# Kernel optimization log

Hardware: AMD Instinct MI355X
Metric: run time of the kernel (lower is better)

The kernel has to match this reference:

```python
import jax, jax.numpy as jnp
from jax import lax
import numpy as np

STATE_DIM = 64
CHANNELS = 128
SEQ_LEN = 4096
BATCH = 16
DT_MIN, DT_MAX = 1e-3, 1e-1


def hippo(n):
    # HiPPO-LegS construction, matching the torch staticmethod
    ar = jnp.arange(n, dtype=jnp.float32)
    P = jnp.sqrt(1.0 + 2.0 * ar)
    A = P[:, None] * P[None, :]
    A = jnp.tril(A) - jnp.diag(ar)
    B = jnp.sqrt(2.0 * ar + 1.0)
    return -A, B[:, None]


def setup_inputs() -> dict:
    key = jax.random.key(0)
    k_u, k_c = jax.random.split(key)
    A, B = hippo(STATE_DIM)
    # xavier_normal_ for C: std = sqrt(2/(fan_in+fan_out))
    std = float(np.sqrt(2.0 / (CHANNELS + STATE_DIM)))
    C = jax.random.normal(k_c, (CHANNELS, STATE_DIM), dtype=jnp.float32) * std
    D = jnp.ones((CHANNELS, 1), dtype=jnp.float32)
    # deterministic dt at log-midpoint of [dt_min, dt_max]
    dt = jnp.exp(jnp.array([(np.log(DT_MIN) + np.log(DT_MAX)) / 2.0], dtype=jnp.float32))
    u = jax.random.normal(k_u, (BATCH, SEQ_LEN), dtype=jnp.float32)
    return {"u": u, "A": A, "B": B, "C": C, "D": D, "dt": dt}


def reference(u, A, B, C, D, dt):
    # Training-path forward of LinearStateSpaceLayer (conv-kernel construction + conv1d)
    b, L = u.shape
    n = A.shape[0]
    dt_s = dt[0]
    I = jnp.eye(n, dtype=A.dtype)
    BL = jnp.linalg.inv(I - 0.5 * dt_s * A)            # bilinear discretization
    A_bar = BL @ (I + 0.5 * dt_s * A)                  # (n, n)
    B_bar = (BL * dt_s) @ B                            # (n, 1)

    # kernel k[j] = C @ A_bar^j @ B_bar for j = 0..L-1, via a scan of matvecs
    def step(v, _):
        return A_bar @ v, v
    _, vs = lax.scan(step, B_bar[:, 0], None, length=L)  # (L, n), vs[j] = A_bar^j B_bar
    k_causal = vs @ C.T                                  # (L, channels)
    # torch ordering: k_conv[c, 0, i] = C A_bar^{L-1-i} B_bar = k_causal[L-1-i, c]
    k_conv = k_causal[::-1].T[:, None, :]                # (channels, 1, L)

    # torch F.conv1d is cross-correlation; lax conv_general_dilated matches
    y = lax.conv_general_dilated(
        u[:, None, :], k_conv,
        window_strides=(1,), padding=[(L - 1, L - 1)],
        dimension_numbers=("NCH", "OIH", "NCH"),
    )[:, :, :L]                                          # (b, channels, L)

    # skip term: (u.unsqueeze(-1) @ D.T).transpose(-1,-2) == u[b,t] * D[c,0]
    y = y + u[:, None, :] * D[None, :, :]                # (b, channels, L)
    return y
```

## Files before the change

kernel.cpp:

```cpp
#include <hip/hip_runtime.h>

#define NS   64
#define CH   128
#define LSEQ 4096
#define NB   16
#define SCH  64
#define MCH  64
#define ST   68
#define CP   128

#define WS_ABAR 0
#define WS_A16  4096
#define WS_VS   8192
#define WS_BBAR 12288

#define X0_IDX(b, m) (((size_t)(b) * CH) * LSEQ + (size_t)(m) * SCH)

#define P_VSS  0
#define P_XCW  1024
#define P_XBS  1280
#define P_PLE  1536
#define P_PART 1792
#define P_A16  2048

#define FMA44(av, bv)                                                          \
    a0.x += av.x * bv.x; a0.y += av.x * bv.y; a0.z += av.x * bv.z; a0.w += av.x * bv.w; \
    a1.x += av.y * bv.x; a1.y += av.y * bv.y; a1.z += av.y * bv.z; a1.w += av.y * bv.w; \
    a2.x += av.z * bv.x; a2.y += av.z * bv.y; a2.z += av.z * bv.z; a2.w += av.z * bv.w; \
    a3.x += av.w * bv.x; a3.y += av.w * bv.y; a3.z += av.w * bv.z; a3.w += av.w * bv.w;


template<bool WT>
__device__ __forceinline__ void mm_square(const float* __restrict__ cm,
                                          const float* __restrict__ cmt,
                                          float* __restrict__ nm,
                                          float* __restrict__ nmt, int e) {
    const int l = e & 63;
    const int si0 = 16 * ((e >> 6) & 3) + 4 * (l >> 4);
    const int sj0 = 4 * (l & 15);
    const int kmax = si0 + 4;
    float4 a0 = {0,0,0,0}, a1 = {0,0,0,0}, a2 = {0,0,0,0}, a3 = {0,0,0,0};
    for (int k = 0; k < kmax; k += 4) {
        float4 av0 = *(const float4*)&cmt[(k + 0) * ST + si0];
        float4 bv0 = *(const float4*)&cm [(k + 0) * ST + sj0];
        float4 av1 = *(const float4*)&cmt[(k + 1) * ST + si0];
        float4 bv1 = *(const float4*)&cm [(k + 1) * ST + sj0];
        float4 av2 = *(const float4*)&cmt[(k + 2) * ST + si0];
        float4 bv2 = *(const float4*)&cm [(k + 2) * ST + sj0];
        float4 av3 = *(const float4*)&cmt[(k + 3) * ST + si0];
        float4 bv3 = *(const float4*)&cm [(k + 3) * ST + sj0];
        FMA44(av0, bv0)
        FMA44(av1, bv1)
        FMA44(av2, bv2)
        FMA44(av3, bv3)
    }
    *(float4*)&nm[(si0 + 0) * ST + sj0] = a0;
    *(float4*)&nm[(si0 + 1) * ST + sj0] = a1;
    *(float4*)&nm[(si0 + 2) * ST + sj0] = a2;
    *(float4*)&nm[(si0 + 3) * ST + sj0] = a3;
    if (WT) {
        float4 t0 = {a0.x, a1.x, a2.x, a3.x};
        float4 t1 = {a0.y, a1.y, a2.y, a3.y};
        float4 t2 = {a0.z, a1.z, a2.z, a3.z};
        float4 t3 = {a0.w, a1.w, a2.w, a3.w};
        *(float4*)&nmt[(sj0 + 0) * ST + si0] = t0;
        *(float4*)&nmt[(sj0 + 1) * ST + si0] = t1;
        *(float4*)&nmt[(sj0 + 2) * ST + si0] = t2;
        *(float4*)&nmt[(sj0 + 3) * ST + si0] = t3;
    }
}

__device__ __forceinline__ void mm_sq42(const float* __restrict__ cm,
                                        const float* __restrict__ cmt,
                                        float* __restrict__ nm,
                                        float* __restrict__ nmt, int tid) {
    const int si0 = 4 * (tid >> 5);
    const int sj0 = 2 * (tid & 31);
    const int kmax = si0 + 4;
    float2 a0 = {0,0}, a1 = {0,0}, a2 = {0,0}, a3 = {0,0};
#pragma unroll 4
    for (int k = 0; k < kmax; ++k) {
        float4 av = *(const float4*)&cmt[k * ST + si0];
        float2 bv = *(const float2*)&cm [k * ST + sj0];
        a0.x += av.x * bv.x; a0.y += av.x * bv.y;
        a1.x += av.y * bv.x; a1.y += av.y * bv.y;
        a2.x += av.z * bv.x; a2.y += av.z * bv.y;
        a3.x += av.w * bv.x; a3.y += av.w * bv.y;
    }
    *(float2*)&nm[(si0 + 0) * ST + sj0] = a0;
    *(float2*)&nm[(si0 + 1) * ST + sj0] = a1;
    *(float2*)&nm[(si0 + 2) * ST + sj0] = a2;
    *(float2*)&nm[(si0 + 3) * ST + sj0] = a3;
    float4 t0 = {a0.x, a1.x, a2.x, a3.x};
    float4 t1 = {a0.y, a1.y, a2.y, a3.y};
    *(float4*)&nmt[(sj0 + 0) * ST + si0] = t0;
    *(float4*)&nmt[(sj0 + 1) * ST + si0] = t1;
}

__device__ __forceinline__ void vs_expand1(const float* __restrict__ cmt,
                                           float* __restrict__ VT,
                                           int iq, int j, int mexp) {
    const int i0 = 4 * iq;
    float4 acc = {0,0,0,0};
#pragma unroll 8
    for (int k = 0; k < NS; ++k) {
        float4 av = *(const float4*)&cmt[k * ST + i0];
        float bk = VT[k * ST + j];
        acc.x += av.x * bk; acc.y += av.y * bk;
        acc.z += av.z * bk; acc.w += av.w * bk;
    }
    VT[(i0 + 0) * ST + mexp + j] = acc.x;
    VT[(i0 + 1) * ST + mexp + j] = acc.y;
    VT[(i0 + 2) * ST + mexp + j] = acc.z;
    VT[(i0 + 3) * ST + mexp + j] = acc.w;
}

__device__ __forceinline__ void pq_step(const float* __restrict__ Acol,
                                        const float* __restrict__ xle,
                                        float* __restrict__ outb, int r0, int e) {
    const int g = e >> 4, i0 = 4 * (e & 15);
    const float* bp = &xle[(4 * g + r0) * NS];
    float4 acc = *(const float4*)&xle[(4 * g + r0 + 1) * NS + i0];
#pragma unroll 8
    for (int k = 0; k < NS; ++k) {
        float4 av = *(const float4*)&Acol[k * ST + i0];
        float bk = bp[k];
        acc.x = fmaf(av.x, bk, acc.x); acc.y = fmaf(av.y, bk, acc.y);
        acc.z = fmaf(av.z, bk, acc.z); acc.w = fmaf(av.w, bk, acc.w);
    }
    *(float4*)&outb[g * ST + i0] = acc;
}

__device__ __forceinline__ void y_step512(const float* __restrict__ A128col,
                                          const float* __restrict__ P,
                                          const float* __restrict__ Q,
                                          float* __restrict__ Y, int e) {
    const int g = e >> 5, c0 = 2 * (e & 31);
    const float* bp = &P[g * ST];
    float2 acc = *(const float2*)&Q[g * ST + c0];
#pragma unroll 8
    for (int k = 0; k < NS; ++k) {
        float2 av = *(const float2*)&A128col[k * ST + c0];
        float bk = bp[k];
        acc.x = fmaf(av.x, bk, acc.x); acc.y = fmaf(av.y, bk, acc.y);
    }
    *(float2*)&Y[g * ST + c0] = acc;
}

__device__ __forceinline__ void inner_step(const float* __restrict__ Acol,
                                           const float* __restrict__ xle,
                                           float* __restrict__ stash, int r, int e) {
    const int g = e >> 4, i0 = 4 * (e & 15);
    const int mp = 4 * g + r - 1;
    float4 acc = *(const float4*)&xle[mp * NS + i0];
    const float* xp = &stash[mp * ST];
#pragma unroll 8
    for (int k = 0; k < NS; ++k) {
        float4 av = *(const float4*)&Acol[k * ST + i0];
        float xk = xp[k];
        acc.x = fmaf(av.x, xk, acc.x); acc.y = fmaf(av.y, xk, acc.y);
        acc.z = fmaf(av.z, xk, acc.z); acc.w = fmaf(av.w, xk, acc.w);
    }
    *(float4*)&stash[(mp + 1) * ST + i0] = acc;
}

__device__ __forceinline__ void inner512(const float* __restrict__ Acol,
                                         const float* __restrict__ xle,
                                         float* __restrict__ stash, int r, int e) {
    const int g = e >> 5, c0 = 2 * (e & 31);
    const int mp = 4 * g + r - 1;
    float2 acc = *(const float2*)&xle[mp * NS + c0];
    const float* xp = &stash[mp * ST];
#pragma unroll 8
    for (int k = 0; k < NS; ++k) {
        float2 av = *(const float2*)&Acol[k * ST + c0];
        float xk = xp[k];
        acc.x = fmaf(av.x, xk, acc.x); acc.y = fmaf(av.y, xk, acc.y);
    }
    *(float2*)&stash[(mp + 1) * ST + c0] = acc;
}

__device__ __forceinline__ void e1u_step(const float* __restrict__ A128col,
                                         const float* __restrict__ P,
                                         float* __restrict__ stash, int e) {
    const int g = e >> 4, i0 = 4 * (e & 15);
    const float* xp = &stash[(4 * g) * ST];
    float4 acc = *(const float4*)&P[g * ST + i0];
#pragma unroll 8
    for (int k = 0; k < NS; ++k) {
        float4 av = *(const float4*)&A128col[k * ST + i0];
        float xk = xp[k];
        acc.x = fmaf(av.x, xk, acc.x); acc.y = fmaf(av.y, xk, acc.y);
        acc.z = fmaf(av.z, xk, acc.z); acc.w = fmaf(av.w, xk, acc.w);
    }
    *(float4*)&stash[(4 * g + 2) * ST + i0] = acc;
}

__global__ __launch_bounds__(512) void k_sb(const float* __restrict__ u,
                                            const float* __restrict__ A,
                                            const float* __restrict__ Bv,
                                            const float* __restrict__ dtp,
                                            float* __restrict__ ws,
                                            float* __restrict__ out) {
    __shared__ __align__(16) float Mrow[NS * ST];
    __shared__ __align__(16) float Mcol[(NS + 1) * ST];
    __shared__ __align__(16) float Nrow[NS * ST];
    __shared__ __align__(16) float Ncol[NS * ST];
    __shared__ __align__(16) float VT[NS * ST];
    __shared__ __align__(16) float uT[NS * ST];
    __shared__ __align__(16) float vsS[NS * NS];
    __shared__ __align__(16) float xleS[MCH * NS];
    __shared__ __align__(16) float bcol[NS];
    __shared__ float rdiag[NS], xcS[NS];
    float* const stash = uT;
    float* const HbP = vsS;
    float* const HbQ = vsS + 16 * ST;
    float* const HbY = vsS + 32 * ST;
    const int tid = threadIdx.x;
    const int b = blockIdx.x;
    const float dt = dtp[0];
    const float hdt = 0.5f * dt;

    for (int o = tid; o < NS * NS; o += 512) {
        int i = o >> 6, k = o & 63;
        float a = A[o];
        float d = (i == k) ? 1.0f : 0.0f;
        Nrow[i * ST + k] = d - hdt * a;
        Ncol[k * ST + i] = d + hdt * a;
    }
    if (tid < NS) {
        bcol[tid]  = dt * Bv[tid];
        rdiag[tid] = 1.0f / (1.0f - hdt * A[tid * NS + tid]);
    }
    __syncthreads();

    {
        const int jj = tid & 63;
#pragma unroll
        for (int rep = 0; rep < 2; ++rep) {
            const int m0 = 4 * (tid >> 6) + 32 * rep;
            float4 v;
            v.x = u[b * LSEQ + (m0 + 0) * SCH + 63 - jj];
            v.y = u[b * LSEQ + (m0 + 1) * SCH + 63 - jj];
            v.z = u[b * LSEQ + (m0 + 2) * SCH + 63 - jj];
            v.w = u[b * LSEQ + (m0 + 3) * SCH + 63 - jj];
            *(float4*)&uT[jj * ST + m0] = v;
        }
    }

    if (tid <= NS) {
        float xr[NS];
        const float* t2b = (tid < NS) ? &Ncol[tid * ST] : bcol;
#pragma unroll
        for (int I = 0; I < 16; ++I) {
            const int i0 = 4 * I;
            float4 t2 = *(const float4*)&t2b[i0];
            float a0 = t2.x, a1 = t2.y, a2 = t2.z, a3 = t2.w;
#pragma unroll
            for (int k = 0; k < i0; k += 4) {
                float4 n0 = *(const float4*)&Nrow[(i0 + 0) * ST + k];
                float4 n1 = *(const float4*)&Nrow[(i0 + 1) * ST + k];
                float4 n2 = *(const float4*)&Nrow[(i0 + 2) * ST + k];
                float4 n3 = *(const float4*)&Nrow[(i0 + 3) * ST + k];
                a0 -= n0.x * xr[k] + n0.y * xr[k + 1] + n0.z * xr[k + 2] + n0.w * xr[k + 3];
                a1 -= n1.x * xr[k] + n1.y * xr[k + 1] + n1.z * xr[k + 2] + n1.w * xr[k + 3];
                a2 -= n2.x * xr[k] + n2.y * xr[k + 1] + n2.z * xr[k + 2] + n2.w * xr[k + 3];
                a3 -= n3.x * xr[k] + n3.y * xr[k + 1] + n3.z * xr[k + 2] + n3.w * xr[k + 3];
            }
            float4 rd  = *(const float4*)&rdiag[i0];
            float4 nb1 = *(const float4*)&Nrow[(i0 + 1) * ST + i0];
            float4 nb2 = *(const float4*)&Nrow[(i0 + 2) * ST + i0];
            float4 nb3 = *(const float4*)&Nrow[(i0 + 3) * ST + i0];
            float x0 = a0 * rd.x;
            float x1 = (a1 - nb1.x * x0) * rd.y;
            float x2 = (a2 - nb2.x * x0 - nb2.y * x1) * rd.z;
            float x3 = (a3 - nb3.x * x0 - nb3.y * x1 - nb3.z * x2) * rd.w;
            xr[i0 + 0] = x0; xr[i0 + 1] = x1; xr[i0 + 2] = x2; xr[i0 + 3] = x3;
        }
        float* xrow = &Mcol[tid * ST];
#pragma unroll
        for (int k = 0; k < NS; k += 4) {
            float4 v = {xr[k], xr[k + 1], xr[k + 2], xr[k + 3]};
            *(float4*)&xrow[k] = v;
        }
    }
    __syncthreads();

    if (tid < 256) {
        const int i0 = 4 * (tid >> 4), j0 = 4 * (tid & 15);
        float4 r0 = *(const float4*)&Mcol[(j0 + 0) * ST + i0];
        float4 r1 = *(const float4*)&Mcol[(j0 + 1) * ST + i0];
        float4 r2 = *(const float4*)&Mcol[(j0 + 2) * ST + i0];
        float4 r3 = *(const float4*)&Mcol[(j0 + 3) * ST + i0];
        float4 w0 = {r0.x, r1.x, r2.x, r3.x};
        float4 w1 = {r0.y, r1.y, r2.y, r3.y};
        float4 w2 = {r0.z, r1.z, r2.z, r3.z};
        float4 w3 = {r0.w, r1.w, r2.w, r3.w};
        *(float4*)&Mrow[(i0 + 0) * ST + j0] = w0;
        *(float4*)&Mrow[(i0 + 1) * ST + j0] = w1;
        *(float4*)&Mrow[(i0 + 2) * ST + j0] = w2;
        *(float4*)&Mrow[(i0 + 3) * ST + j0] = w3;
        if (b == 0) {
            *(float4*)&ws[WS_ABAR + (i0 + 0) * NS + j0] = w0;
            *(float4*)&ws[WS_ABAR + (i0 + 1) * NS + j0] = w1;
            *(float4*)&ws[WS_ABAR + (i0 + 2) * NS + j0] = w2;
            *(float4*)&ws[WS_ABAR + (i0 + 3) * NS + j0] = w3;
        }
    }
    if (b == 1 && tid < 16)
        *(float4*)&ws[WS_BBAR + 4 * tid] = *(const float4*)&Mcol[NS * ST + 4 * tid];
    if (tid < NS) VT[tid * ST + 0] = Mcol[NS * ST + tid];
    __syncthreads();

    float *cm = Mrow, *cmt = Mcol, *nm = Nrow, *nmt = Ncol;
    for (int s = 1; s <= 6; ++s) {
        if (s <= 4) {
            mm_sq42(cm, cmt, nm, nmt, tid);
            const int mexp = 1 << (s - 1);
            if (tid < 16 * mexp) {
                vs_expand1(cmt, VT, tid & 15, tid >> 4, mexp);
            }
        } else if (tid < 256) {
            mm_square<true>(cm, cmt, nm, nmt, tid);
        } else {
            const int e = tid - 256;
            const int iq = e & 15;
            if (s == 5) {
                vs_expand1(cmt, VT, iq, e >> 4, 16);
            } else {
                const int j0 = 2 * (e >> 4);
                const int i0 = 4 * iq;
                float4 c0 = {0,0,0,0}, c1 = {0,0,0,0};
#pragma unroll 8
                for (int k = 0; k < NS; ++k) {
                    float4 av = *(const float4*)&cmt[k * ST + i0];
                    float2 bv = *(const float2*)&VT[k * ST + j0];
                    c0.x += av.x * bv.x; c0.y += av.y * bv.x;
                    c0.z += av.z * bv.x; c0.w += av.w * bv.x;
                    c1.x += av.x * bv.y; c1.y += av.y * bv.y;
                    c1.z += av.z * bv.y; c1.w += av.w * bv.y;
                }
                float2 w0 = {c0.x, c1.x}, w1 = {c0.y, c1.y};
                float2 w2 = {c0.z, c1.z}, w3 = {c0.w, c1.w};
                *(float2*)&VT[(i0 + 0) * ST + 32 + j0] = w0;
                *(float2*)&VT[(i0 + 1) * ST + 32 + j0] = w1;
                *(float2*)&VT[(i0 + 2) * ST + 32 + j0] = w2;
                *(float2*)&VT[(i0 + 3) * ST + 32 + j0] = w3;
            }
        }
        __syncthreads();
        { float* t = cm; cm = nm; nm = t; t = cmt; cmt = nmt; nmt = t; }
        if (s == 4 && b == 2) {
            for (int o = tid; o < (NS * NS) / 4; o += 512) {
                int r = o >> 4, c4 = (o & 15) * 4;
                *(float4*)&ws[WS_A16 + r * NS + c4] = *(const float4*)&cm[r * ST + c4];
            }
        }
    }

    if (tid < 256) {
        const int i0 = 4 * (tid >> 4), j0 = 4 * (tid & 15);
        float4 v0 = *(const float4*)&VT[(i0 + 0) * ST + j0];
        float4 v1 = *(const float4*)&VT[(i0 + 1) * ST + j0];
        float4 v2 = *(const float4*)&VT[(i0 + 2) * ST + j0];
        float4 v3 = *(const float4*)&VT[(i0 + 3) * ST + j0];
        float4 w0 = {v0.x, v1.x, v2.x, v3.x};
        float4 w1 = {v0.y, v1.y, v2.y, v3.y};
        float4 w2 = {v0.z, v1.z, v2.z, v3.z};
        float4 w3 = {v0.w, v1.w, v2.w, v3.w};
        *(float4*)&vsS[(j0 + 0) * NS + i0] = w0;
        *(float4*)&vsS[(j0 + 1) * NS + i0] = w1;
        *(float4*)&vsS[(j0 + 2) * NS + i0] = w2;
        *(float4*)&vsS[(j0 + 3) * NS + i0] = w3;
        if (b == 3) {
            *(float4*)&ws[WS_VS + (j0 + 0) * NS + i0] = w0;
            *(float4*)&ws[WS_VS + (j0 + 1) * NS + i0] = w1;
            *(float4*)&ws[WS_VS + (j0 + 2) * NS + i0] = w2;
            *(float4*)&ws[WS_VS + (j0 + 3) * NS + i0] = w3;
        }
    } else {
        mm_square<true>(Mrow, Mcol, Nrow, Ncol, tid - 256);
    }
    __syncthreads();

    if (tid < 256) {
        const int ig = tid & 15, mg = tid >> 4;
        float4 a0 = {0,0,0,0}, a1 = {0,0,0,0}, a2 = {0,0,0,0}, a3 = {0,0,0,0};
#pragma unroll 4
        for (int j = 0; j < NS; j += 2) {
            float4 am  = *(const float4*)&uT[j * ST + 4 * mg];
            float4 bi  = *(const float4*)&vsS[j * NS + 4 * ig];
            float4 am2 = *(const float4*)&uT[(j + 1) * ST + 4 * mg];
            float4 bi2 = *(const float4*)&vsS[(j + 1) * NS + 4 * ig];
            FMA44(am, bi)
            FMA44(am2, bi2)
        }
        *(float4*)&xleS[(4 * mg + 0) * NS + 4 * ig] = a0;
        *(float4*)&xleS[(4 * mg + 1) * NS + 4 * ig] = a1;
        *(float4*)&xleS[(4 * mg + 2) * NS + 4 * ig] = a2;
        *(float4*)&xleS[(4 * mg + 3) * NS + 4 * ig] = a3;
    } else {
        mm_square<false>(Nrow, Ncol, VT, VT, tid - 256);
    }
    __syncthreads();

    if (tid < 256) pq_step(Mcol, xleS, HbP, 0, tid);
    else           pq_step(Mcol, xleS, HbQ, 2, tid - 256);
    if (tid < 64) { xcS[tid] = 0.f; stash[tid] = 0.f; }
    __syncthreads();

    y_step512(Ncol, HbP, HbQ, HbY, tid);
    __syncthreads();

    if (tid < 64) {
        const int i = tid;
        float4 arow[16];
#pragma unroll
        for (int c = 0; c < 16; ++c)
            arow[c] = *(const float4*)&VT[i * ST + 4 * c];
        float yv[15];
#pragma unroll
        for (int g = 0; g < 15; ++g) yv[g] = HbY[g * ST + i];
        for (int g = 0; g < 15; ++g) {
            float a0 = 0.f, a1 = 0.f, a2 = 0.f, a3 = 0.f;
#pragma unroll
            for (int c = 0; c < 16; ++c) {
                float4 xv = *(const float4*)&xcS[4 * c];
                a0 = fmaf(arow[c].x, xv.x, a0);
                a1 = fmaf(arow[c].y, xv.y, a1);
                a2 = fmaf(arow[c].z, xv.z, a2);
                a3 = fmaf(arow[c].w, xv.w, a3);
            }
            const float xn = ((a0 + a1) + (a2 + a3)) + yv[g];
            xcS[i] = xn;
            stash[(4 * g + 4) * ST + i] = xn;
        }
    }
    __syncthreads();

    if (tid < 256) inner_step(Mcol, xleS, stash, 1, tid);
    else           e1u_step(Ncol, HbP, stash, tid - 256);
    __syncthreads();

    inner512(Mcol, xleS, stash, 3, tid);
    __syncthreads();

    {
        const int m = tid >> 3, t8 = (tid & 7) * 8;
        float4 o1 = *(const float4*)&stash[m * ST + t8];
        float4 o2 = *(const float4*)&stash[m * ST + t8 + 4];
        *(float4*)&out[X0_IDX(b, m) + t8]     = o1;
        *(float4*)&out[X0_IDX(b, m) + t8 + 4] = o2;
    }
}

__global__ __launch_bounds__(256) void k_main2(const float* __restrict__ u,
                                               const float* __restrict__ Cm,
                                               const float* __restrict__ Dv,
                                               const float* __restrict__ ws,
                                               float* __restrict__ out) {
    __shared__ __align__(16) float Xl[NS * ST];
    __shared__ __align__(16) float pool[NS * CP];
    __shared__ float uS[SCH], DS[CH], bbS[NS];
    const int m = blockIdx.x, b = blockIdx.y;
    const int tid = threadIdx.x;
    const int l = tid & 63, w = tid >> 6;

    for (int o = tid; o < (NS * NS) / 4; o += 256) {
        int r = o >> 4, c4 = (o & 15) * 4;
        *(float4*)&Xl[r * ST + c4]          = *(const float4*)&ws[WS_ABAR + r * NS + c4];
        *(float4*)&pool[P_A16 + r * NS + c4] = *(const float4*)&ws[WS_A16 + r * NS + c4];
    }
    for (int o = tid; o < 16 * NS; o += 256) pool[P_VSS + o] = ws[WS_VS + o];
    if (tid < NS) {
        uS[tid]  = u[b * LSEQ + m * SCH + tid];
        bbS[tid] = ws[WS_BBAR + tid];
        pool[P_XBS + tid] = out[X0_IDX(b, m) + tid];
    }
    if (tid < CH) DS[tid] = Dv[tid];
    __syncthreads();

    float4 arow[16];
#pragma unroll
    for (int c = 0; c < 16; ++c)
        arow[c] = *(const float4*)&Xl[l * ST + 4 * c];
    const float bbl = bbS[l];
    float ur[16];
#pragma unroll
    for (int s = 0; s < 16; ++s) ur[s] = uS[16 * w + s];
    float4 a16r[4];
#pragma unroll
    for (int kq = 0; kq < 4; ++kq)
        a16r[kq] = *(const float4*)&pool[P_A16 + l * NS + 16 * w + 4 * kq];

    {
        float s = 0.f;
#pragma unroll
        for (int j = 0; j < 16; ++j) s += pool[P_VSS + j * NS + l] * uS[16 * w + 15 - j];
        pool[P_PLE + w * NS + l] = s;
    }
    __syncthreads();

    for (int p = 1; p < 4; ++p) {
        float4 x0q = *(const float4*)&pool[P_XBS + (p - 1) * NS + 16 * w + 0];
        float4 x1q = *(const float4*)&pool[P_XBS + (p - 1) * NS + 16 * w + 4];
        float4 x2q = *(const float4*)&pool[P_XBS + (p - 1) * NS + 16 * w + 8];
        float4 x3q = *(const float4*)&pool[P_XBS + (p - 1) * NS + 16 * w + 12];
        float s = a16r[0].x * x0q.x + a16r[0].y * x0q.y + a16r[0].z * x0q.z + a16r[0].w * x0q.w
                + a16r[1].x * x1q.x + a16r[1].y * x1q.y + a16r[1].z * x1q.z + a16r[1].w * x1q.w
                + a16r[2].x * x2q.x + a16r[2].y * x2q.y + a16r[2].z * x2q.z + a16r[2].w * x2q.w
                + a16r[3].x * x3q.x + a16r[3].y * x3q.y + a16r[3].z * x3q.z + a16r[3].w * x3q.w;
        pool[P_PART + w * NS + l] = s;
        __syncthreads();
        if (w == 0) {
            float xn = pool[P_PART + l] + pool[P_PART + NS + l] + pool[P_PART + 2 * NS + l]
                     + pool[P_PART + 3 * NS + l] + pool[P_PLE + (p - 1) * NS + l];
            pool[P_XBS + p * NS + l] = xn;
        }
        __syncthreads();
    }

    pool[P_XCW + w * NS + l] = pool[P_XBS + w * NS + l];
    for (int s = 0; s < 16; ++s) {
        const int t = 16 * w + s;
        float a0 = 0.f, a1 = 0.f, a2 = 0.f, a3 = 0.f;
#pragma unroll
        for (int c = 0; c < 16; ++c) {
            float4 xv = *(const float4*)&pool[P_XCW + w * NS + 4 * c];
            a0 = fmaf(arow[c].x, xv.x, a0);
            a1 = fmaf(arow[c].y, xv.y, a1);
            a2 = fmaf(arow[c].z, xv.z, a2);
            a3 = fmaf(arow[c].w, xv.w, a3);
        }
        const float xn = ((a0 + a1) + (a2 + a3)) + bbl * ur[s];
        pool[P_XCW + w * NS + l] = xn;
        Xl[l * ST + t] = xn;
    }
    __syncthreads();

#pragma unroll
    for (int rep = 0; rep < 8; ++rep) {
        const int ii = tid & 63;
        const int cg = (tid >> 6) + 4 * rep;
        float4 v;
        v.x = Cm[(4 * cg + 0) * NS + ii];
        v.y = Cm[(4 * cg + 1) * NS + ii];
        v.z = Cm[(4 * cg + 2) * NS + ii];
        v.w = Cm[(4 * cg + 3) * NS + ii];
        *(float4*)&pool[ii * CP + 4 * cg] = v;
    }
    __syncthreads();

    {
        const int tg = tid & 7, cq = tid >> 3;
        float acc[4][8];
#pragma unroll
        for (int r = 0; r < 4; ++r)
#pragma unroll
            for (int c = 0; c < 8; ++c) acc[r][c] = 0.f;
#pragma unroll 4
        for (int ii = 0; ii < NS; ++ii) {
            float4 cv = *(const float4*)&pool[ii * CP + 4 * cq];
            float4 xa = *(const float4*)&Xl[ii * ST + 8 * tg + 0];
            float4 xb = *(const float4*)&Xl[ii * ST + 8 * tg + 4];
            float cr[4] = {cv.x, cv.y, cv.z, cv.w};
            float xv[8] = {xa.x, xa.y, xa.z, xa.w, xb.x, xb.y, xb.z, xb.w};
#pragma unroll
            for (int r = 0; r < 4; ++r)
#pragma unroll
                for (int c = 0; c < 8; ++c) acc[r][c] += cr[r] * xv[c];
        }
        const size_t obase = ((size_t)b * CH) * LSEQ + (size_t)m * SCH + 8 * tg;
#pragma unroll
        for (int r = 0; r < 4; ++r) {
            const int c = 4 * cq + r;
            const float dv = DS[c];
            float4 o1, o2;
            o1.x = acc[r][0] + dv * uS[8 * tg + 0];
            o1.y = acc[r][1] + dv * uS[8 * tg + 1];
            o1.z = acc[r][2] + dv * uS[8 * tg + 2];
            o1.w = acc[r][3] + dv * uS[8 * tg + 3];
            o2.x = acc[r][4] + dv * uS[8 * tg + 4];
            o2.y = acc[r][5] + dv * uS[8 * tg + 5];
            o2.z = acc[r][6] + dv * uS[8 * tg + 6];
            o2.w = acc[r][7] + dv * uS[8 * tg + 7];
            float* op = out + obase + (size_t)c * LSEQ;
            *(float4*)(op)     = o1;
            *(float4*)(op + 4) = o2;
        }
    }
}

extern "C" void kernel_launch(void* const* d_in, const int* in_sizes, int n_in,
                              void* d_out, int out_size, void* d_ws, size_t ws_size,
                              hipStream_t stream) {
    const float* u   = (const float*)d_in[0];
    const float* A   = (const float*)d_in[1];
    const float* Bv  = (const float*)d_in[2];
    const float* Cm  = (const float*)d_in[3];
    const float* Dv  = (const float*)d_in[4];
    const float* dtp = (const float*)d_in[5];
    float* ws  = (float*)d_ws;
    float* out = (float*)d_out;

    k_sb<<<NB, 512, 0, stream>>>(u, A, Bv, dtp, ws, out);
    k_main2<<<dim3(MCH, NB), 256, 0, stream>>>(u, Cm, Dv, ws, out);
}
```

Measured before the change: 149.4 us.

## Process two sequence chunks per block in main kernel to amortize setup

Each k_main2 block now handles two consecutive 64-step chunks instead of one, with a second LDS state buffer, and the grid is halved. The per-block setup work (loading A_bar, A^16, the VS table and the transposed C matrix into shared memory) is paid once for two chunks. The cost is half as many blocks (512 instead of 1024), which lowers parallelism and latency hiding, and the two chunks' sequential recurrences run back to back inside each block. Extra LDS may also reduce occupancy.

Result: faster. 145.8 us, median of 2 (-2.5%).

```diff
diff --git a/kernel.cpp b/kernel.cpp
--- a/kernel.cpp
+++ b/kernel.cpp
@@ -459,23 +459,25 @@
                                                const float* __restrict__ Dv,
                                                const float* __restrict__ ws,
                                                float* __restrict__ out) {
-    __shared__ __align__(16) float Xl[NS * ST];
+    __shared__ __align__(16) float Xl [NS * ST];
+    __shared__ __align__(16) float Xl2[NS * ST];
     __shared__ __align__(16) float pool[NS * CP];
-    __shared__ float uS[SCH], DS[CH], bbS[NS];
-    const int m = blockIdx.x, b = blockIdx.y;
+    __shared__ float uS[2][SCH], DS[CH], bbS[NS];
+    const int mq = blockIdx.x, b = blockIdx.y;
+    const int m0 = 2 * mq;
     const int tid = threadIdx.x;
     const int l = tid & 63, w = tid >> 6;
 
     for (int o = tid; o < (NS * NS) / 4; o += 256) {
         int r = o >> 4, c4 = (o & 15) * 4;
-        *(float4*)&Xl[r * ST + c4]          = *(const float4*)&ws[WS_ABAR + r * NS + c4];
+        *(float4*)&Xl[r * ST + c4]           = *(const float4*)&ws[WS_ABAR + r * NS + c4];
         *(float4*)&pool[P_A16 + r * NS + c4] = *(const float4*)&ws[WS_A16 + r * NS + c4];
     }
     for (int o = tid; o < 16 * NS; o += 256) pool[P_VSS + o] = ws[WS_VS + o];
     if (tid < NS) {
-        uS[tid]  = u[b * LSEQ + m * SCH + tid];
-        bbS[tid] = ws[WS_BBAR + tid];
-        pool[P_XBS + tid] = out[X0_IDX(b, m) + tid];
+        uS[0][tid] = u[b * LSEQ + (m0 + 0) * SCH + tid];
+        uS[1][tid] = u[b * LSEQ + (m0 + 1) * SCH + tid];
+        bbS[tid]   = ws[WS_BBAR + tid];
     }
     if (tid < CH) DS[tid] = Dv[tid];
     __syncthreads();
@@ -485,58 +487,64 @@
     for (int c = 0; c < 16; ++c)
         arow[c] = *(const float4*)&Xl[l * ST + 4 * c];
     const float bbl = bbS[l];
-    float ur[16];
-#pragma unroll
-    for (int s = 0; s < 16; ++s) ur[s] = uS[16 * w + s];
     float4 a16r[4];
 #pragma unroll
     for (int kq = 0; kq < 4; ++kq)
         a16r[kq] = *(const float4*)&pool[P_A16 + l * NS + 16 * w + 4 * kq];
 
-    {
-        float s = 0.f;
-#pragma unroll
-        for (int j = 0; j < 16; ++j) s += pool[P_VSS + j * NS + l] * uS[16 * w + 15 - j];
-        pool[P_PLE + w * NS + l] = s;
-    }
-    __syncthreads();
-
-    for (int p = 1; p < 4; ++p) {
-        float4 x0q = *(const float4*)&pool[P_XBS + (p - 1) * NS + 16 * w + 0];
-        float4 x1q = *(const float4*)&pool[P_XBS + (p - 1) * NS + 16 * w + 4];
-        float4 x2q = *(const float4*)&pool[P_XBS + (p - 1) * NS + 16 * w + 8];
-        float4 x3q = *(const float4*)&pool[P_XBS + (p - 1) * NS + 16 * w + 12];
-        float s = a16r[0].x * x0q.x + a16r[0].y * x0q.y + a16r[0].z * x0q.z + a16r[0].w * x0q.w
-                + a16r[1].x * x1q.x + a16r[1].y * x1q.y + a16r[1].z * x1q.z + a16r[1].w * x1q.w
-                + a16r[2].x * x2q.x + a16r[2].y * x2q.y + a16r[2].z * x2q.z + a16r[2].w * x2q.w
-                + a16r[3].x * x3q.x + a16r[3].y * x3q.y + a16r[3].z * x3q.z + a16r[3].w * x3q.w;
-        pool[P_PART + w * NS + l] = s;
+    for (int c = 0; c < 2; ++c) {
+        const int m = m0 + c;
+        float* const Xp = c ? Xl2 : Xl;
+
+        {
+            float s = 0.f;
+#pragma unroll
+            for (int j = 0; j < 16; ++j) s += pool[P_VSS + j * NS + l] * uS[c][16 * w + 15 - j];
+            pool[P_PLE + w * NS + l] = s;
+        }
+        if (tid < NS) pool[P_XBS + tid] = out[X0_IDX(b, m) + tid];
         __syncthreads();
-        if (w == 0) {
-            float xn = pool[P_PART + l] + pool[P_PART + NS + l] + pool[P_PART + 2 * NS + l]
-                     + pool[P_PART + 3 * NS + l] + pool[P_PLE + (p - 1) * NS + l];
-            pool[P_XBS + p * NS + l] = xn;
+
+        for (int p = 1; p < 4; ++p) {
+            float4 x0q = *(const float4*)&pool[P_XBS + (p - 1) * NS + 16 * w + 0];
+            float4 x1q = *(const float4*)&pool[P_XBS + (p - 1) * NS + 16 * w + 4];
+            float4 x2q = *(const float4*)&pool[P_XBS + (p - 1) * NS + 16 * w + 8];
+            float4 x3q = *(const float4*)&pool[P_XBS + (p - 1) * NS + 16 * w + 12];
+            float s = a16r[0].x * x0q.x + a16r[0].y * x0q.y + a16r[0].z * x0q.z + a16r[0].w * x0q.w
+                    + a16r[1].x * x1q.x + a16r[1].y * x1q.y + a16r[1].z * x1q.z + a16r[1].w * x1q.w
+                    + a16r[2].x * x2q.x + a16r[2].y * x2q.y + a16r[2].z * x2q.z + a16r[2].w * x2q.w
+                    + a16r[3].x * x3q.x + a16r[3].y * x3q.y + a16r[3].z * x3q.z + a16r[3].w * x3q.w;
+            pool[P_PART + w * NS + l] = s;
+            __syncthreads();
+            if (w == 0) {
+                float xn = pool[P_PART + l] + pool[P_PART + NS + l] + pool[P_PART + 2 * NS + l]
+                         + pool[P_PART + 3 * NS + l] + pool[P_PLE + (p - 1) * NS + l];
+                pool[P_XBS + p * NS + l] = xn;
+            }
+            __syncthreads();
+        }
+
+        float ur[16];
+#pragma unroll
+        for (int s = 0; s < 16; ++s) ur[s] = uS[c][16 * w + s];
+        pool[P_XCW + w * NS + l] = pool[P_XBS + w * NS + l];
+        for (int s = 0; s < 16; ++s) {
+            const int t = 16 * w + s;
+            float a0 = 0.f, a1 = 0.f, a2 = 0.f, a3 = 0.f;
+#pragma unroll
+            for (int cc = 0; cc < 16; ++cc) {
+                float4 xv = *(const float4*)&pool[P_XCW + w * NS + 4 * cc];
+                a0 = fmaf(arow[cc].x, xv.x, a0);
+                a1 = fmaf(arow[cc].y, xv.y, a1);
+                a2 = fmaf(arow[cc].z, xv.z, a2);
+                a3 = fmaf(arow[cc].w, xv.w, a3);
+            }
+            const float xn = ((a0 + a1) + (a2 + a3)) + bbl * ur[s];
+            pool[P_XCW + w * NS + l] = xn;
+            Xp[l * ST + t] = xn;
         }
         __syncthreads();
     }
-
-    pool[P_XCW + w * NS + l] = pool[P_XBS + w * NS + l];
-    for (int s = 0; s < 16; ++s) {
-        const int t = 16 * w + s;
-        float a0 = 0.f, a1 = 0.f, a2 = 0.f, a3 = 0.f;
-#pragma unroll
-        for (int c = 0; c < 16; ++c) {
-            float4 xv = *(const float4*)&pool[P_XCW + w * NS + 4 * c];
-            a0 = fmaf(arow[c].x, xv.x, a0);
-            a1 = fmaf(arow[c].y, xv.y, a1);
-            a2 = fmaf(arow[c].z, xv.z, a2);
-            a3 = fmaf(arow[c].w, xv.w, a3);
-        }
-        const float xn = ((a0 + a1) + (a2 + a3)) + bbl * ur[s];
-        pool[P_XCW + w * NS + l] = xn;
-        Xl[l * ST + t] = xn;
-    }
-    __syncthreads();
 
 #pragma unroll
     for (int rep = 0; rep < 8; ++rep) {
@@ -551,40 +559,41 @@
     }
     __syncthreads();
 
-    {
+    for (int c = 0; c < 2; ++c) {
+        const float* const Xp = c ? Xl2 : Xl;
         const int tg = tid & 7, cq = tid >> 3;
         float acc[4][8];
 #pragma unroll
         for (int r = 0; r < 4; ++r)
 #pragma unroll
-            for (int c = 0; c < 8; ++c) acc[r][c] = 0.f;
+            for (int cc = 0; cc < 8; ++cc) acc[r][cc] = 0.f;
 #pragma unroll 4
         for (int ii = 0; ii < NS; ++ii) {
             float4 cv = *(const float4*)&pool[ii * CP + 4 * cq];
-            float4 xa = *(const float4*)&Xl[ii * ST + 8 * tg + 0];
-            float4 xb = *(const float4*)&Xl[ii * ST + 8 * tg + 4];
+            float4 xa = *(const float4*)&Xp[ii * ST + 8 * tg + 0];
+            float4 xb = *(const float4*)&Xp[ii * ST + 8 * tg + 4];
             float cr[4] = {cv.x, cv.y, cv.z, cv.w};
             float xv[8] = {xa.x, xa.y, xa.z, xa.w, xb.x, xb.y, xb.z, xb.w};
 #pragma unroll
             for (int r = 0; r < 4; ++r)
 #pragma unroll
-                for (int c = 0; c < 8; ++c) acc[r][c] += cr[r] * xv[c];
-        }
-        const size_t obase = ((size_t)b * CH) * LSEQ + (size_t)m * SCH + 8 * tg;
+                for (int cc = 0; cc < 8; ++cc) acc[r][cc] += cr[r] * xv[cc];
+        }
+        const size_t obase = ((size_t)b * CH) * LSEQ + (size_t)(m0 + c) * SCH + 8 * tg;
 #pragma unroll
         for (int r = 0; r < 4; ++r) {
-            const int c = 4 * cq + r;
-            const float dv = DS[c];
+            const int ch = 4 * cq + r;
+            const float dv = DS[ch];
             float4 o1, o2;
-            o1.x = acc[r][0] + dv * uS[8 * tg + 0];
-            o1.y = acc[r][1] + dv * uS[8 * tg + 1];
-            o1.z = acc[r][2] + dv * uS[8 * tg + 2];
-            o1.w = acc[r][3] + dv * uS[8 * tg + 3];
-            o2.x = acc[r][4] + dv * uS[8 * tg + 4];
-            o2.y = acc[r][5] + dv * uS[8 * tg + 5];
-            o2.z = acc[r][6] + dv * uS[8 * tg + 6];
-            o2.w = acc[r][7] + dv * uS[8 * tg + 7];
-            float* op = out + obase + (size_t)c * LSEQ;
+            o1.x = acc[r][0] + dv * uS[c][8 * tg + 0];
+            o1.y = acc[r][1] + dv * uS[c][8 * tg + 1];
+            o1.z = acc[r][2] + dv * uS[c][8 * tg + 2];
+            o1.w = acc[r][3] + dv * uS[c][8 * tg + 3];
+            o2.x = acc[r][4] + dv * uS[c][8 * tg + 4];
+            o2.y = acc[r][5] + dv * uS[c][8 * tg + 5];
+            o2.z = acc[r][6] + dv * uS[c][8 * tg + 6];
+            o2.w = acc[r][7] + dv * uS[c][8 * tg + 7];
+            float* op = out + obase + (size_t)ch * LSEQ;
             *(float4*)(op)     = o1;
             *(float4*)(op + 4) = o2;
         }
@@ -604,5 +613,5 @@
     float* out = (float*)d_out;
 
     k_sb<<<NB, 512, 0, stream>>>(u, A, Bv, dtp, ws, out);
-    k_main2<<<dim3(MCH, NB), 256, 0, stream>>>(u, Cm, Dv, ws, out);
-}
+    k_main2<<<dim3(MCH / 2, NB), 256, 0, stream>>>(u, Cm, Dv, ws, out);
+}
```
